# Kernel optimization log

Hardware: AMD Instinct MI355X
Metric: run time of the kernel (lower is better)

The kernel has to match this reference:

```python
import jax, jax.numpy as jnp
import numpy as np

B, S, D_MODEL = 1, 2048, 2048
N_HEADS, N_KV_HEADS, D_HEAD = 16, 4, 128
ROTARY_DIM, ROTARY_BASE = 128, 10000.0
ATTN_SCALE = float(np.sqrt(D_HEAD))
REPEAT = N_HEADS // N_KV_HEADS


def _sin_cos_rotary(n_ctx, rotary_dim, base):
    # TransformerLens calculate_sin_cos_rotary, rotary_adjacent_pairs=False:
    # freq repeated as 'd -> (2 d)'
    pos = jnp.arange(n_ctx, dtype=jnp.float32)
    dim = jnp.arange(rotary_dim // 2, dtype=jnp.float32)
    freq = base ** (dim / (rotary_dim / 2))
    freq = jnp.concatenate([freq, freq])  # (2 d)
    angles = pos[:, None] / freq[None, :]  # [n_ctx, rotary_dim]
    return jnp.sin(angles), jnp.cos(angles)


def _rotate_every_two_half(x):
    # rotate_half for non-adjacent pairs: [-x2, x1]
    d = x.shape[-1]
    return jnp.concatenate([-x[..., d // 2:], x[..., : d // 2]], axis=-1)


def _apply_rotary(x, sin, cos):
    # x: [batch, pos, head, d_head]; sin/cos: [n_ctx, rotary_dim]
    p = x.shape[1]
    s = sin[:p][:, None, :]  # [pos, 1, rotary_dim]
    c = cos[:p][:, None, :]
    x_rot = x[..., :ROTARY_DIM]
    x_pass = x[..., ROTARY_DIM:]
    x_rotated = x_rot * c + _rotate_every_two_half(x_rot) * s
    return jnp.concatenate([x_rotated, x_pass], axis=-1)


def setup_inputs() -> dict:
    key = jax.random.key(0)
    ks = jax.random.split(key, 10)
    init = 1.0 / np.sqrt(D_MODEL)
    return {
        "query_input": jax.random.normal(ks[0], (B, S, D_MODEL), jnp.float32),
        "key_input": jax.random.normal(ks[1], (B, S, D_MODEL), jnp.float32),
        "value_input": jax.random.normal(ks[2], (B, S, D_MODEL), jnp.float32),
        "W_Q": jax.random.normal(ks[3], (N_HEADS, D_MODEL, D_HEAD), jnp.float32) * init,
        "b_Q": jnp.zeros((N_HEADS, D_HEAD), jnp.float32),
        "W_K": jax.random.normal(ks[4], (N_KV_HEADS, D_MODEL, D_HEAD), jnp.float32) * init,
        "b_K": jnp.zeros((N_KV_HEADS, D_HEAD), jnp.float32),
        "W_V": jax.random.normal(ks[5], (N_KV_HEADS, D_MODEL, D_HEAD), jnp.float32) * init,
        "b_V": jnp.zeros((N_KV_HEADS, D_HEAD), jnp.float32),
        "W_O": jax.random.normal(ks[6], (N_HEADS, D_HEAD, D_MODEL), jnp.float32) * init,
        "b_O": jnp.zeros((D_MODEL,), jnp.float32),
    }


def reference(query_input, key_input, value_input, W_Q, b_Q, W_K, b_K, W_V, b_V, W_O, b_O):
    sin, cos = _sin_cos_rotary(S, ROTARY_DIM, ROTARY_BASE)

    # Projections
    q = jnp.einsum("bpd,hdk->bphk", query_input, W_Q) + b_Q   # [B,S,H,dh]
    k = jnp.einsum("bpd,hdk->bphk", key_input, W_K) + b_K     # [B,S,Hkv,dh]
    v = jnp.einsum("bpd,hdk->bphk", value_input, W_V) + b_V   # [B,S,Hkv,dh]

    # Rotary on q and k (before KV head expansion)
    q = _apply_rotary(q, sin, cos)
    k = _apply_rotary(k, sin, cos)

    # GQA expansion via repeat_interleave on head dim
    k = jnp.repeat(k, REPEAT, axis=2)  # [B,S,H,dh]
    v = jnp.repeat(v, REPEAT, axis=2)

    # Attention scores, causal mask, softmax
    scores = jnp.einsum("bqhd,bkhd->bhqk", q, k) / ATTN_SCALE  # [B,H,S,S]
    causal = jnp.tril(jnp.ones((S, S), dtype=bool))
    scores = jnp.where(causal, scores, jnp.finfo(scores.dtype).min)
    pattern = jax.nn.softmax(scores, axis=-1)

    # Weighted values and output projection
    z = jnp.einsum("bhqk,bkhd->bqhd", pattern, v)              # [B,S,H,dh]
    out = jnp.einsum("bqhd,hdm->bqm", z, W_O) + b_O            # [B,S,D]
    return out
```

## Files before the change

### kernel.cpp

```cpp
#include <hip/hip_runtime.h>
#include <hip/hip_bf16.h>
#include <stdint.h>
#include <math.h>

typedef __bf16 bf16_t;
typedef __attribute__((ext_vector_type(8))) __bf16 bf16x8;
typedef __attribute__((ext_vector_type(4))) __bf16 bf16x4;
typedef __attribute__((ext_vector_type(4))) float f32x4;
typedef __attribute__((ext_vector_type(16))) float f32x16;
typedef unsigned int uint2v __attribute__((ext_vector_type(2)));

static constexpr int S = 2048;
static constexpr int DM = 2048;
static constexpr int NH = 16;
static constexpr int NKV = 4;
static constexpr int DH = 128;

#define MFMA16(a, b, c) __builtin_amdgcn_mfma_f32_16x16x32_bf16((a), (b), (c), 0, 0, 0)
#define MFMA32(a, b, c) __builtin_amdgcn_mfma_f32_32x32x16_bf16((a), (b), (c), 0, 0, 0)

__device__ __forceinline__ void gload_lds16(const void* g, void* l) {
  __builtin_amdgcn_global_load_lds((__attribute__((address_space(1))) void*)(g),
                                   (__attribute__((address_space(3))) void*)(l), 16, 0, 0);
}

template <int N>
__device__ __forceinline__ void wait_vmcnt() {
  asm volatile("s_waitcnt vmcnt(%0)" :: "n"(N) : "memory");
}
__device__ __forceinline__ void wait_lgkm0() {
  asm volatile("s_waitcnt lgkmcnt(0)" ::: "memory");
}

__device__ __forceinline__ unsigned cvtpk(float lo, float hi) {
  unsigned r;
  asm("v_cvt_pk_bf16_f32 %0, %1, %2" : "=v"(r) : "v"(lo), "v"(hi));
  return r;
}
__device__ __forceinline__ void plswap2(unsigned& a, unsigned& b) {
  uint2v r = __builtin_amdgcn_permlane32_swap(a, b, false, false);
  a = r[0]; b = r[1];
}
__device__ __forceinline__ float swapred_max(float x) {
  uint2v r = __builtin_amdgcn_permlane32_swap(__float_as_uint(x), __float_as_uint(x), false, false);
  return fmaxf(__uint_as_float(r[0]), __uint_as_float(r[1]));
}
__device__ __forceinline__ float swapred_sum(float x) {
  uint2v r = __builtin_amdgcn_permlane32_swap(__float_as_uint(x), __float_as_uint(x), false, false);
  return __uint_as_float(r[0]) + __uint_as_float(r[1]);
}
__device__ __forceinline__ bf16x8 packfrag(float a0, float a1, float a2, float a3,
                                           float a4, float a5, float a6, float a7) {
  unsigned w0 = cvtpk(a0, a1), w1 = cvtpk(a2, a3);
  unsigned w2 = cvtpk(a4, a5), w3 = cvtpk(a6, a7);
  plswap2(w0, w2); plswap2(w1, w3);
  union { unsigned u[4]; bf16x8 v; } u;
  u.u[0] = w0; u.u[1] = w1; u.u[2] = w2; u.u[3] = w3;
  return u.v;
}

__device__ const unsigned char attn_map[51] = {
  120,121,122,123,124, 112,113,114,115,116, 104,105,106,107, 96,97,98,99,
  88,89,90,91, 80,81,82, 72,73,74, 64,65,66, 56,57, 48,49, 40,41, 32, 24, 16,
  108, 83, 58, 33, 8, 125, 100, 75, 50, 25, 0};
__device__ const unsigned char sbase[16] = {0,0,0,0,2,4,6,9,12,15,19,23,27,32,37,42};

__global__ __launch_bounds__(256)
void prep_k(const float* __restrict__ Xq, const float* __restrict__ Xk,
            const float* __restrict__ Xv, const float* __restrict__ WQ,
            const float* __restrict__ WK, const float* __restrict__ WV,
            const float* __restrict__ WO, float2* __restrict__ tab,
            bf16_t* __restrict__ xq, bf16_t* __restrict__ xk, bf16_t* __restrict__ xv,
            bf16_t* __restrict__ wqT, bf16_t* __restrict__ wkT, bf16_t* __restrict__ wvT,
            bf16_t* __restrict__ woT) {
  __shared__ float tile[32][33];
  const int b = blockIdx.x, t = threadIdx.x;
  if (b < 512) {
    int idx = b * 256 + t;
    int p = idx >> 6, j = idx & 63;
    double inv = exp2(-(double)j * 13.287712379549449 / 64.0);
    double ang = (double)p * inv;
    tab[idx] = make_float2((float)sin(ang), (float)cos(ang));
  } else if (b < 12800) {
    int i = ((b - 512) * 256 + t) * 4;
    const float* in; bf16_t* out; int off;
    if (i < 4194304) { in = Xq; out = xq; off = i; }
    else if (i < 8388608) { in = Xk; out = xk; off = i - 4194304; }
    else { in = Xv; out = xv; off = i - 8388608; }
    f32x4 v = *(const f32x4*)(in + off);
    bf16x4 o;
    o[0] = (bf16_t)v[0]; o[1] = (bf16_t)v[1]; o[2] = (bf16_t)v[2]; o[3] = (bf16_t)v[3];
    *(bf16x4*)(out + off) = o;
  } else if (b < 16896) {
    int b2 = b - 12800;
    int bx = b2 & 3, by = (b2 >> 2) & 63, bz = b2 >> 8;
    int c0 = bx * 32, r0 = by * 32;
    int tx = t & 31, ty = t >> 5;
    const float* src = WQ + (size_t)bz * 2048 * 128;
    #pragma unroll
    for (int j = 0; j < 32; j += 8)
      tile[ty + j][tx] = src[(size_t)(r0 + ty + j) * 128 + c0 + tx];
    __syncthreads();
    #pragma unroll
    for (int j = 0; j < 32; j += 8)
      wqT[(size_t)(bz * 128 + c0 + ty + j) * 2048 + r0 + tx] = (bf16_t)tile[tx][ty + j];
  } else if (b < 18944) {
    int b2 = b - 16896;
    int bx = b2 & 3, by = (b2 >> 2) & 63, bz = b2 >> 8;
    int g = bz & 3;
    const float* in = (bz < 4) ? WK : WV;
    bf16_t* out = (bz < 4) ? wkT : wvT;
    int c0 = bx * 32, r0 = by * 32;
    int tx = t & 31, ty = t >> 5;
    const float* src = in + (size_t)g * 2048 * 128;
    #pragma unroll
    for (int j = 0; j < 32; j += 8)
      tile[ty + j][tx] = src[(size_t)(r0 + ty + j) * 128 + c0 + tx];
    __syncthreads();
    #pragma unroll
    for (int j = 0; j < 32; j += 8)
      out[(size_t)(g * 128 + c0 + ty + j) * 2048 + r0 + tx] = (bf16_t)tile[tx][ty + j];
  } else {
    int b2 = b - 18944;
    int bx = b2 & 63, by = (b2 >> 6) & 3, bz = b2 >> 8;
    int c0 = bx * 32, r0 = by * 32;
    int tx = t & 31, ty = t >> 5;
    const float* src = WO + (size_t)bz * 128 * 2048;
    #pragma unroll
    for (int j = 0; j < 32; j += 8)
      tile[ty + j][tx] = src[(size_t)(r0 + ty + j) * 2048 + c0 + tx];
    __syncthreads();
    #pragma unroll
    for (int j = 0; j < 32; j += 8)
      woT[(size_t)(c0 + ty + j) * 2048 + bz * 128 + r0 + tx] = (bf16_t)tile[tx][ty + j];
  }
}

__global__ __launch_bounds__(256)
void proj_gemm_k(const bf16_t* __restrict__ xq, const bf16_t* __restrict__ xk,
                 const bf16_t* __restrict__ xv, const bf16_t* __restrict__ wqT,
                 const bf16_t* __restrict__ wkT, const bf16_t* __restrict__ wvT,
                 const float* __restrict__ bQ, const float* __restrict__ bK,
                 const float* __restrict__ bV, const float2* __restrict__ tab,
                 float qscale, bf16_t* __restrict__ Qb,
                 bf16_t* __restrict__ Kb, bf16_t* __restrict__ Vt) {
  const int b = blockIdx.x;
  const int xcd = b & 7, idx = b >> 3;
  const int nb = (xcd & 3) * 12 + idx % 12;
  const int m0 = ((xcd >> 2) * 8 + idx / 12) * 128;
  const bf16_t* A; const bf16_t* B; const float* bias; bf16_t* dst;
  int ncol0 = 0, hbase = 0, hb = 0;
  float scale = 1.0f;
  bool vmode = false;
  if (nb < 32)      { A = xq; B = wqT; bias = bQ; dst = Qb; hbase = (nb >> 1) * 128; hb = nb & 1; scale = qscale; }
  else if (nb < 40) { A = xk; B = wkT; bias = bK; dst = Kb; hbase = ((nb - 32) >> 1) * 128; hb = (nb - 32) & 1; }
  else              { A = xv; B = wvT; bias = bV; dst = Vt; ncol0 = (nb - 40) * 64; vmode = true; }
  const int K = 2048;
  const int t = threadIdx.x;
  const int lane = t & 63, w = t >> 6;
  const int l15 = lane & 15, lg = lane >> 4;
  const int wr = (w >> 1) * 64, wc = (w & 1) * 32;

  __shared__ bf16_t lA[2][128 * 64];
  __shared__ bf16_t lB[2][64 * 64];

  f32x4 acc[4][2] = {};
  const int srow = t >> 3;
  const int sslot = t & 7;

  auto stage = [&](int buf, int kt) {
    #pragma unroll
    for (int i = 0; i < 4; ++i) {
      int row = i * 32 + srow;
      int ss = sslot ^ (row & 7);
      gload_lds16(A + (size_t)(m0 + row) * K + kt * 64 + ss * 8,
                  (void*)(&lA[buf][0] + i * 2048 + t * 8));
    }
    #pragma unroll
    for (int i = 0; i < 2; ++i) {
      int row = i * 32 + srow;
      int ss = sslot ^ (row & 7);
      int grow = vmode ? (ncol0 + row)
                       : (hbase + hb * 32 + (row >> 1) + 64 * (row & 1));
      gload_lds16(B + (size_t)grow * K + kt * 64 + ss * 8,
                  (void*)(&lB[buf][0] + i * 2048 + t * 8));
    }
  };

  const int nk = K >> 6;
  stage(0, 0);
  for (int kt = 0; kt < nk; ++kt) {
    const int cur = kt & 1;
    if (kt + 1 < nk) {
      stage(cur ^ 1, kt + 1);
      wait_vmcnt<6>();
    } else {
      wait_vmcnt<0>();
    }
    __builtin_amdgcn_s_barrier();
    #pragma unroll
    for (int kk = 0; kk < 2; ++kk) {
      bf16x8 af[4], bfv[2];
      #pragma unroll
      for (int f = 0; f < 4; ++f) {
        int row = wr + f * 16 + l15;
        int slot = kk * 4 + lg;
        af[f] = *(const bf16x8*)(&lA[cur][0] + row * 64 + ((slot ^ (row & 7)) * 8));
      }
      #pragma unroll
      for (int f = 0; f < 2; ++f) {
        int row = wc + f * 16 + l15;
        int slot = kk * 4 + lg;
        bfv[f] = *(const bf16x8*)(&lB[cur][0] + row * 64 + ((slot ^ (row & 7)) * 8));
      }
      #pragma unroll
      for (int fm = 0; fm < 4; ++fm)
        #pragma unroll
        for (int fn = 0; fn < 2; ++fn)
          acc[fm][fn] = MFMA16(af[fm], bfv[fn], acc[fm][fn]);
    }
    wait_lgkm0();
    __builtin_amdgcn_s_barrier();
  }

  if (vmode) {
    #pragma unroll
    for (int fm = 0; fm < 4; ++fm) {
      int rowb = m0 + wr + fm * 16 + lg * 4;
      #pragma unroll
      for (int fn = 0; fn < 2; ++fn) {
        int col = ncol0 + wc + fn * 16 + l15;
        float bb = bias[col];
        bf16x4 pk;
        #pragma unroll
        for (int r = 0; r < 4; ++r) pk[r] = (bf16_t)(acc[fm][fn][r] + bb);
        *(bf16x4*)(dst + (size_t)col * S + rowb) = pk;
      }
    }
  } else {
    #pragma unroll
    for (int fm = 0; fm < 4; ++fm) {
      int rowb = m0 + wr + fm * 16 + lg * 4;
      #pragma unroll
      for (int fn = 0; fn < 2; ++fn) {
        int tc = wc + fn * 16 + l15;
        int j = hb * 32 + (tc >> 1);
        int half = tc & 1;
        int col = hbase + j + 64 * half;
        float bb = bias[col];
        #pragma unroll
        for (int r = 0; r < 4; ++r) {
          int rr = rowb + r;
          float v = acc[fm][fn][r] + bb;
          float o = __shfl_xor(v, 1);
          float2 sc = tab[rr * 64 + j];
          float res = half ? (v * sc.y + o * sc.x) : (v * sc.y - o * sc.x);
          dst[((size_t)(col >> 7) * S + rr) * DH + (col & 127)] = (bf16_t)(res * scale);
        }
      }
    }
  }
}

__global__ __launch_bounds__(256)
void gemm_o_k(const bf16_t* __restrict__ A, const bf16_t* __restrict__ B,
              const float* __restrict__ bias, float* __restrict__ Cout) {
  const int b = blockIdx.x;
  const int xcd = b & 7, idx = b >> 3;
  const int ncol0 = ((xcd & 3) * 8 + (idx & 7)) * 64;
  const int m0 = (((xcd >> 2) * 8) + (idx >> 3)) * 128;
  const int K = 2048;
  const int t = threadIdx.x;
  const int lane = t & 63, w = t >> 6;
  const int l15 = lane & 15, lg = lane >> 4;
  const int wr = (w >> 1) * 64, wc = (w & 1) * 32;

  __shared__ bf16_t lA[2][128 * 64];
  __shared__ bf16_t lB[2][64 * 64];

  f32x4 acc[4][2] = {};
  const int srow = t >> 3;
  const int sslot = t & 7;

  auto stage = [&](int buf, int kt) {
    #pragma unroll
    for (int i = 0; i < 4; ++i) {
      int row = i * 32 + srow;
      int ss = sslot ^ (row & 7);
      gload_lds16(A + (size_t)(m0 + row) * K + kt * 64 + ss * 8,
                  (void*)(&lA[buf][0] + i * 2048 + t * 8));
    }
    #pragma unroll
    for (int i = 0; i < 2; ++i) {
      int row = i * 32 + srow;
      int ss = sslot ^ (row & 7);
      gload_lds16(B + (size_t)(ncol0 + row) * K + kt * 64 + ss * 8,
                  (void*)(&lB[buf][0] + i * 2048 + t * 8));
    }
  };

  const int nk = K >> 6;
  stage(0, 0);
  for (int kt = 0; kt < nk; ++kt) {
    const int cur = kt & 1;
    if (kt + 1 < nk) {
      stage(cur ^ 1, kt + 1);
      wait_vmcnt<6>();
    } else {
      wait_vmcnt<0>();
    }
    __builtin_amdgcn_s_barrier();
    #pragma unroll
    for (int kk = 0; kk < 2; ++kk) {
      bf16x8 af[4], bfv[2];
      #pragma unroll
      for (int f = 0; f < 4; ++f) {
        int row = wr + f * 16 + l15;
        int slot = kk * 4 + lg;
        af[f] = *(const bf16x8*)(&lA[cur][0] + row * 64 + ((slot ^ (row & 7)) * 8));
      }
      #pragma unroll
      for (int f = 0; f < 2; ++f) {
        int row = wc + f * 16 + l15;
        int slot = kk * 4 + lg;
        bfv[f] = *(const bf16x8*)(&lB[cur][0] + row * 64 + ((slot ^ (row & 7)) * 8));
      }
      #pragma unroll
      for (int fm = 0; fm < 4; ++fm)
        #pragma unroll
        for (int fn = 0; fn < 2; ++fn)
          acc[fm][fn] = MFMA16(af[fm], bfv[fn], acc[fm][fn]);
    }
    wait_lgkm0();
    __builtin_amdgcn_s_barrier();
  }

  #pragma unroll
  for (int fm = 0; fm < 4; ++fm) {
    int rowb = m0 + wr + fm * 16 + lg * 4;
    #pragma unroll
    for (int fn = 0; fn < 2; ++fn) {
      int col = ncol0 + wc + fn * 16 + l15;
      float bb = bias[col];
      #pragma unroll
      for (int r = 0; r < 4; ++r)
        Cout[(size_t)(rowb + r) * DM + col] = acc[fm][fn][r] + bb;
    }
  }
}

__global__ __launch_bounds__(256, 2)
void attn_k(const bf16_t* __restrict__ Q, const bf16_t* __restrict__ K,
            const bf16_t* __restrict__ Vt, bf16_t* __restrict__ Z,
            bf16_t* __restrict__ Opart, float* __restrict__ mpart,
            float* __restrict__ lpart) {
  const int bid = blockIdx.x;
  const int h = bid & 15;
  const int g = bid >> 4;
  const int code = attn_map[g];
  const int qb = code >> 3, ci = code & 7;
  const bool split = qb >= 3;
  const int it0 = 3 * ci;
  const int itend = (3 * ci + 2 < qb) ? (3 * ci + 2) : qb;
  const int q0 = qb * 128;
  const int hkv = h >> 2;
  const int t = threadIdx.x;
  const int lane = t & 63, w = t >> 6;
  const int l31 = lane & 31, hi = lane >> 5;
  const int qrow = q0 + w * 32 + l31;

  __shared__ bf16_t lK[128 * 128];
  __shared__ bf16_t lV[128 * 128];

  bf16x8 qf[8];
  #pragma unroll
  for (int j = 0; j < 8; ++j)
    qf[j] = *(const bf16x8*)(Q + ((size_t)h * S + qrow) * DH + j * 16 + hi * 8);

  auto stageK = [&](int it) {
    #pragma unroll
    for (int i = 0; i < 8; ++i) {
      int row = i * 16 + (t >> 4);
      int ss = (t & 15) ^ (row & 15);
      gload_lds16(K + ((size_t)hkv * S + it * 128 + row) * DH + ss * 8,
                  (void*)(lK + i * 2048 + t * 8));
    }
  };
  auto stageV = [&](int it) {
    #pragma unroll
    for (int i = 0; i < 8; ++i) {
      int row = i * 16 + (t >> 4);
      int ss = (t & 15) ^ (row & 15);
      gload_lds16(Vt + ((size_t)hkv * DH + row) * S + it * 128 + ss * 8,
                  (void*)(lV + i * 2048 + t * 8));
    }
  };

  f32x16 oacc0 = {}, oacc1 = {}, oacc2 = {}, oacc3 = {};
  float m_run = -3.0e3f, l_run = 0.f;
  const int msk = l31 & 15;
  const bf16_t* kb0 = lK + l31 * 128;
  const bf16_t* vb0 = lV + l31 * 128;

  stageK(it0);
  stageV(it0);

  for (int it = it0; it <= itend; ++it) {
    wait_vmcnt<8>();
    __builtin_amdgcn_s_barrier();

    f32x16 s0 = {}, s1 = {}, s2 = {}, s3 = {};
    __builtin_amdgcn_s_setprio(1);
    #pragma unroll
    for (int j = 0; j < 8; ++j) {
      int so = ((j * 2 + hi) ^ msk) * 8;
      bf16x8 k0 = *(const bf16x8*)(kb0 + so);
      bf16x8 k1 = *(const bf16x8*)(kb0 + 32 * 128 + so);
      bf16x8 k2 = *(const bf16x8*)(kb0 + 64 * 128 + so);
      bf16x8 k3 = *(const bf16x8*)(kb0 + 96 * 128 + so);
      s0 = MFMA32(k0, qf[j], s0);
      s1 = MFMA32(k1, qf[j], s1);
      s2 = MFMA32(k2, qf[j], s2);
      s3 = MFMA32(k3, qf[j], s3);
    }
    __builtin_amdgcn_s_setprio(0);
    wait_lgkm0();
    __builtin_amdgcn_s_barrier();
    if (it < itend) stageK(it + 1);

    if (it == qb) {
#define MASKG(SN, N) { \
      _Pragma("unroll") \
      for (int r = 0; r < 16; ++r) { \
        int key = it * 128 + (N) * 32 + (r & 3) + 8 * (r >> 2) + 4 * hi; \
        if (key > qrow) SN[r] = -1e30f; \
      } }
      MASKG(s0, 0) MASKG(s1, 1) MASKG(s2, 2) MASKG(s3, 3)
#undef MASKG
    }

    float mxa = fmaxf(fmaxf(s0[0], s1[0]), fmaxf(s2[0], s3[0]));
    float mxb = fmaxf(fmaxf(s0[1], s1[1]), fmaxf(s2[1], s3[1]));
    float mxc = fmaxf(fmaxf(s0[2], s1[2]), fmaxf(s2[2], s3[2]));
    float mxd = fmaxf(fmaxf(s0[3], s1[3]), fmaxf(s2[3], s3[3]));
    #pragma unroll
    for (int r = 4; r < 16; r += 4) {
      mxa = fmaxf(fmaxf(mxa, fmaxf(s0[r], s1[r])), fmaxf(s2[r], s3[r]));
      mxb = fmaxf(fmaxf(mxb, fmaxf(s0[r+1], s1[r+1])), fmaxf(s2[r+1], s3[r+1]));
      mxc = fmaxf(fmaxf(mxc, fmaxf(s0[r+2], s1[r+2])), fmaxf(s2[r+2], s3[r+2]));
      mxd = fmaxf(fmaxf(mxd, fmaxf(s0[r+3], s1[r+3])), fmaxf(s2[r+3], s3[r+3]));
    }
    float mfull = swapred_max(fmaxf(fmaxf(mxa, mxb), fmaxf(mxc, mxd)));

    float m_new, alpha;
    bool nore = __all(mfull - m_run <= 8.0f);
    if (nore) { m_new = m_run; alpha = 1.0f; }
    else { m_new = fmaxf(m_run, mfull); alpha = exp2f(m_run - m_new); }

    float psa = 0.f, psb = 0.f, psc = 0.f, psd = 0.f;
#define EXPG(SN) { \
    _Pragma("unroll") \
    for (int r = 0; r < 16; r += 4) { \
      SN[r] = exp2f(SN[r] - m_new); psa += SN[r]; \
      SN[r+1] = exp2f(SN[r+1] - m_new); psb += SN[r+1]; \
      SN[r+2] = exp2f(SN[r+2] - m_new); psc += SN[r+2]; \
      SN[r+3] = exp2f(SN[r+3] - m_new); psd += SN[r+3]; \
    } }
    EXPG(s0) EXPG(s1) EXPG(s2) EXPG(s3)
#undef EXPG
    float lt = swapred_sum((psa + psb) + (psc + psd));
    l_run = l_run * alpha + lt;
    m_run = m_new;

    if (!nore) {
      #pragma unroll
      for (int r = 0; r < 16; ++r) {
        int qs = (r & 3) + 8 * (r >> 2) + 4 * hi;
        float ar = __shfl(alpha, qs);
        oacc0[r] *= ar; oacc1[r] *= ar; oacc2[r] *= ar; oacc3[r] *= ar;
      }
    }

    bf16x8 pa[8];
    pa[0] = packfrag(s0[0], s0[1], s0[2], s0[3], s0[4], s0[5], s0[6], s0[7]);
    pa[1] = packfrag(s0[8], s0[9], s0[10], s0[11], s0[12], s0[13], s0[14], s0[15]);
    pa[2] = packfrag(s1[0], s1[1], s1[2], s1[3], s1[4], s1[5], s1[6], s1[7]);
    pa[3] = packfrag(s1[8], s1[9], s1[10], s1[11], s1[12], s1[13], s1[14], s1[15]);
    pa[4] = packfrag(s2[0], s2[1], s2[2], s2[3], s2[4], s2[5], s2[6], s2[7]);
    pa[5] = packfrag(s2[8], s2[9], s2[10], s2[11], s2[12], s2[13], s2[14], s2[15]);
    pa[6] = packfrag(s3[0], s3[1], s3[2], s3[3], s3[4], s3[5], s3[6], s3[7]);
    pa[7] = packfrag(s3[8], s3[9], s3[10], s3[11], s3[12], s3[13], s3[14], s3[15]);

    if (it < itend) { wait_vmcnt<8>(); }
    else            { wait_vmcnt<0>(); }
    __builtin_amdgcn_s_barrier();

    __builtin_amdgcn_s_setprio(1);
    #pragma unroll
    for (int ks = 0; ks < 8; ++ks) {
      int so = ((ks * 2 + hi) ^ msk) * 8;
      bf16x8 v0 = *(const bf16x8*)(vb0 + so);
      bf16x8 v1 = *(const bf16x8*)(vb0 + 32 * 128 + so);
      bf16x8 v2 = *(const bf16x8*)(vb0 + 64 * 128 + so);
      bf16x8 v3 = *(const bf16x8*)(vb0 + 96 * 128 + so);
      oacc0 = MFMA32(pa[ks], v0, oacc0);
      oacc1 = MFMA32(pa[ks], v1, oacc1);
      oacc2 = MFMA32(pa[ks], v2, oacc2);
      oacc3 = MFMA32(pa[ks], v3, oacc3);
    }
    __builtin_amdgcn_s_setprio(0);
    wait_lgkm0();
    __builtin_amdgcn_s_barrier();
    if (it < itend) stageV(it + 1);
  }

  if (!split) {
    float linv = 1.0f / l_run;
    #pragma unroll
    for (int r = 0; r < 16; ++r) {
      int qs = (r & 3) + 8 * (r >> 2) + 4 * hi;
      float lv = __shfl(linv, qs);
      int qg = q0 + w * 32 + qs;
      bf16_t* zp = Z + (size_t)qg * DM + h * DH + l31;
      zp[0]  = (bf16_t)(oacc0[r] * lv);
      zp[32] = (bf16_t)(oacc1[r] * lv);
      zp[64] = (bf16_t)(oacc2[r] * lv);
      zp[96] = (bf16_t)(oacc3[r] * lv);
    }
  } else {
    const int slot = h * 48 + sbase[qb] + ci;
    bf16_t* Op = Opart + (size_t)slot * 16384;
    #pragma unroll
    for (int r = 0; r < 16; ++r) {
      int qs = (r & 3) + 8 * (r >> 2) + 4 * hi;
      bf16_t* op = Op + (w * 32 + qs) * 128 + l31;
      op[0]  = (bf16_t)oacc0[r];
      op[32] = (bf16_t)oacc1[r];
      op[64] = (bf16_t)oacc2[r];
      op[96] = (bf16_t)oacc3[r];
    }
    if (lane < 32) {
      mpart[slot * 128 + w * 32 + l31] = m_run;
      lpart[slot * 128 + w * 32 + l31] = l_run;
    }
  }
}

__global__ void combine_k(const bf16_t* __restrict__ Opart, const float* __restrict__ mpart,
                          const float* __restrict__ lpart, bf16_t* __restrict__ Z) {
  int tid = blockIdx.x * 256 + threadIdx.x;
  int d4 = tid & 31;
  int q = (tid >> 5) & 127;
  int u = tid >> 12;
  int h = u / 13;
  int qb = 3 + (u - h * 13);
  int nc = (qb + 3) / 3;
  int slot0 = h * 48 + sbase[qb];
  float M = -3.0e3f;
  for (int c = 0; c < nc; ++c) M = fmaxf(M, mpart[(slot0 + c) * 128 + q]);
  float L = 0.f;
  float o0 = 0.f, o1 = 0.f, o2 = 0.f, o3 = 0.f;
  for (int c = 0; c < nc; ++c) {
    float a = exp2f(mpart[(slot0 + c) * 128 + q] - M);
    L += a * lpart[(slot0 + c) * 128 + q];
    bf16x4 ov = *(const bf16x4*)(Opart + (size_t)(slot0 + c) * 16384 + q * 128 + d4 * 4);
    o0 += a * (float)ov[0]; o1 += a * (float)ov[1];
    o2 += a * (float)ov[2]; o3 += a * (float)ov[3];
  }
  float inv = 1.0f / L;
  bf16x4 zv;
  zv[0] = (bf16_t)(o0 * inv); zv[1] = (bf16_t)(o1 * inv);
  zv[2] = (bf16_t)(o2 * inv); zv[3] = (bf16_t)(o3 * inv);
  int qg = qb * 128 + q;
  *(bf16x4*)(Z + (size_t)qg * DM + h * DH + d4 * 4) = zv;
}

extern "C" void kernel_launch(void* const* d_in, const int* in_sizes, int n_in,
                              void* d_out, int out_size, void* d_ws, size_t ws_size,
                              hipStream_t stream) {
  (void)in_sizes; (void)n_in; (void)out_size; (void)ws_size;
  const float* Xq = (const float*)d_in[0];
  const float* Xk = (const float*)d_in[1];
  const float* Xv = (const float*)d_in[2];
  const float* WQ = (const float*)d_in[3];
  const float* bQ = (const float*)d_in[4];
  const float* WK = (const float*)d_in[5];
  const float* bK = (const float*)d_in[6];
  const float* WV = (const float*)d_in[7];
  const float* bV = (const float*)d_in[8];
  const float* WO = (const float*)d_in[9];
  const float* bO = (const float*)d_in[10];

  char* w = (char*)d_ws;
  float2* tab = (float2*)w;
  bf16_t* xq  = (bf16_t*)(w + (1 << 20));
  bf16_t* xk  = xq + 4194304;
  bf16_t* xv  = xk + 4194304;
  bf16_t* wqT = xv + 4194304;
  bf16_t* wkT = wqT + 4194304;
  bf16_t* wvT = wkT + 1048576;
  bf16_t* woT = wvT + 1048576;
  bf16_t* Qb  = woT + 4194304;
  bf16_t* Kb  = Qb + 4194304;
  bf16_t* Vtb = Kb + 1048576;
  bf16_t* Zb  = Vtb + 1048576;
  bf16_t* Opart = xq;
  float* mpart = (float*)tab;
  float* lpart = mpart + 768 * 128;

  prep_k<<<dim3(23040), dim3(256), 0, stream>>>(Xq, Xk, Xv, WQ, WK, WV, WO, tab,
                                                xq, xk, xv, wqT, wkT, wvT, woT);

  const float qscale = 1.4426950408889634f / sqrtf(128.0f);
  proj_gemm_k<<<dim3(768), dim3(256), 0, stream>>>(xq, xk, xv, wqT, wkT, wvT,
                                                   bQ, bK, bV, tab, qscale,
                                                   Qb, Kb, Vtb);

  attn_k<<<dim3(816), dim3(256), 0, stream>>>(Qb, Kb, Vtb, Zb, Opart, mpart, lpart);
  combine_k<<<dim3(3328), dim3(256), 0, stream>>>(Opart, mpart, lpart, Zb);

  gemm_o_k<<<dim3(512), dim3(256), 0, stream>>>(Zb, woT, bO, (float*)d_out);
}
```

Before: 138.4 us.

## Read K tiles directly from global memory and double-buffer V in LDS

The attention kernel no longer stages K through shared memory. Each wave now loads its K fragments for the QK^T MFMAs straight from global memory into registers. The freed LDS holds a second V buffer, so the next V tile is prefetched into the alternate buffer while the current one is consumed, and most barriers and vmcnt waits are removed. The aim is less LDS traffic and synchronization and better overlap of V loads. In exchange, every wave reads the whole K tile from global memory, which relies on cache hits and exposes load latency with no prefetch of K. Correctness of the V buffer also depends on implicit in-order vmcnt waits from the K loads.

```diff
diff --git a/kernel.cpp b/kernel.cpp
--- a/kernel.cpp
+++ b/kernel.cpp
@@ -369,64 +369,47 @@
   const int l31 = lane & 31, hi = lane >> 5;
   const int qrow = q0 + w * 32 + l31;
 
-  __shared__ bf16_t lK[128 * 128];
-  __shared__ bf16_t lV[128 * 128];
+  __shared__ bf16_t lV[2][128 * 128];
 
   bf16x8 qf[8];
   #pragma unroll
   for (int j = 0; j < 8; ++j)
     qf[j] = *(const bf16x8*)(Q + ((size_t)h * S + qrow) * DH + j * 16 + hi * 8);
 
-  auto stageK = [&](int it) {
-    #pragma unroll
-    for (int i = 0; i < 8; ++i) {
-      int row = i * 16 + (t >> 4);
-      int ss = (t & 15) ^ (row & 15);
-      gload_lds16(K + ((size_t)hkv * S + it * 128 + row) * DH + ss * 8,
-                  (void*)(lK + i * 2048 + t * 8));
-    }
-  };
-  auto stageV = [&](int it) {
+  auto stageV = [&](int buf, int it) {
     #pragma unroll
     for (int i = 0; i < 8; ++i) {
       int row = i * 16 + (t >> 4);
       int ss = (t & 15) ^ (row & 15);
       gload_lds16(Vt + ((size_t)hkv * DH + row) * S + it * 128 + ss * 8,
-                  (void*)(lV + i * 2048 + t * 8));
+                  (void*)(&lV[buf][0] + i * 2048 + t * 8));
     }
   };
 
   f32x16 oacc0 = {}, oacc1 = {}, oacc2 = {}, oacc3 = {};
   float m_run = -3.0e3f, l_run = 0.f;
   const int msk = l31 & 15;
-  const bf16_t* kb0 = lK + l31 * 128;
-  const bf16_t* vb0 = lV + l31 * 128;
-
-  stageK(it0);
-  stageV(it0);
+
+  stageV(0, it0);
 
   for (int it = it0; it <= itend; ++it) {
-    wait_vmcnt<8>();
-    __builtin_amdgcn_s_barrier();
-
+    const int cur = (it - it0) & 1;
+
+    const bf16_t* kp = K + ((size_t)hkv * S + (size_t)it * 128 + l31) * DH + hi * 8;
     f32x16 s0 = {}, s1 = {}, s2 = {}, s3 = {};
     __builtin_amdgcn_s_setprio(1);
     #pragma unroll
     for (int j = 0; j < 8; ++j) {
-      int so = ((j * 2 + hi) ^ msk) * 8;
-      bf16x8 k0 = *(const bf16x8*)(kb0 + so);
-      bf16x8 k1 = *(const bf16x8*)(kb0 + 32 * 128 + so);
-      bf16x8 k2 = *(const bf16x8*)(kb0 + 64 * 128 + so);
-      bf16x8 k3 = *(const bf16x8*)(kb0 + 96 * 128 + so);
+      bf16x8 k0 = *(const bf16x8*)(kp + j * 16);
+      bf16x8 k1 = *(const bf16x8*)(kp + 32 * DH + j * 16);
+      bf16x8 k2 = *(const bf16x8*)(kp + 64 * DH + j * 16);
+      bf16x8 k3 = *(const bf16x8*)(kp + 96 * DH + j * 16);
       s0 = MFMA32(k0, qf[j], s0);
       s1 = MFMA32(k1, qf[j], s1);
       s2 = MFMA32(k2, qf[j], s2);
       s3 = MFMA32(k3, qf[j], s3);
     }
     __builtin_amdgcn_s_setprio(0);
-    wait_lgkm0();
-    __builtin_amdgcn_s_barrier();
-    if (it < itend) stageK(it + 1);
 
     if (it == qb) {
 #define MASKG(SN, N) { \
@@ -481,6 +464,8 @@
       }
     }
 
+    if (it < itend) stageV(cur ^ 1, it + 1);
+
     bf16x8 pa[8];
     pa[0] = packfrag(s0[0], s0[1], s0[2], s0[3], s0[4], s0[5], s0[6], s0[7]);
     pa[1] = packfrag(s0[8], s0[9], s0[10], s0[11], s0[12], s0[13], s0[14], s0[15]);
@@ -491,10 +476,10 @@
     pa[6] = packfrag(s3[0], s3[1], s3[2], s3[3], s3[4], s3[5], s3[6], s3[7]);
     pa[7] = packfrag(s3[8], s3[9], s3[10], s3[11], s3[12], s3[13], s3[14], s3[15]);
 
-    if (it < itend) { wait_vmcnt<8>(); }
-    else            { wait_vmcnt<0>(); }
+    if (it == it0) { wait_vmcnt<8>(); }
     __builtin_amdgcn_s_barrier();
 
+    const bf16_t* vb0 = &lV[cur][0] + l31 * 128;
     __builtin_amdgcn_s_setprio(1);
     #pragma unroll
     for (int ks = 0; ks < 8; ++ks) {
@@ -511,7 +496,6 @@
     __builtin_amdgcn_s_setprio(0);
     wait_lgkm0();
     __builtin_amdgcn_s_barrier();
-    if (it < itend) stageV(it + 1);
   }
 
   if (!split) {
```

After: 166.3 us. 1.2x slower.

## Fuse split-KV combine into attention via last-block atomic counter

Applied to the files above, without the earlier changes.

Removes the separate combine kernel launch. Each split attention block writes its partial output, max and sum, fences, and atomically bumps a per-(head, query-block) counter that prep_k resets. The last block to arrive merges all partials into Z. This saves a launch and the gap between kernels, but adds fences, an atomic and a serial tail of combine work on a few blocks.

```diff
diff --git a/kernel.cpp b/kernel.cpp
--- a/kernel.cpp
+++ b/kernel.cpp
@@ -72,10 +72,11 @@
             const float* __restrict__ WO, float2* __restrict__ tab,
             bf16_t* __restrict__ xq, bf16_t* __restrict__ xk, bf16_t* __restrict__ xv,
             bf16_t* __restrict__ wqT, bf16_t* __restrict__ wkT, bf16_t* __restrict__ wvT,
-            bf16_t* __restrict__ woT) {
+            bf16_t* __restrict__ woT, unsigned* __restrict__ cnt) {
   __shared__ float tile[32][33];
   const int b = blockIdx.x, t = threadIdx.x;
   if (b < 512) {
+    if (b == 0 && t < 208) cnt[t] = 0;
     int idx = b * 256 + t;
     int p = idx >> 6, j = idx & 63;
     double inv = exp2(-(double)j * 13.287712379549449 / 64.0);
@@ -353,7 +354,7 @@
 void attn_k(const bf16_t* __restrict__ Q, const bf16_t* __restrict__ K,
             const bf16_t* __restrict__ Vt, bf16_t* __restrict__ Z,
             bf16_t* __restrict__ Opart, float* __restrict__ mpart,
-            float* __restrict__ lpart) {
+            float* __restrict__ lpart, unsigned* __restrict__ cnt) {
   const int bid = blockIdx.x;
   const int h = bid & 15;
   const int g = bid >> 4;
@@ -527,52 +528,61 @@
       zp[64] = (bf16_t)(oacc2[r] * lv);
       zp[96] = (bf16_t)(oacc3[r] * lv);
     }
-  } else {
-    const int slot = h * 48 + sbase[qb] + ci;
-    bf16_t* Op = Opart + (size_t)slot * 16384;
-    #pragma unroll
-    for (int r = 0; r < 16; ++r) {
-      int qs = (r & 3) + 8 * (r >> 2) + 4 * hi;
-      bf16_t* op = Op + (w * 32 + qs) * 128 + l31;
-      op[0]  = (bf16_t)oacc0[r];
-      op[32] = (bf16_t)oacc1[r];
-      op[64] = (bf16_t)oacc2[r];
-      op[96] = (bf16_t)oacc3[r];
-    }
-    if (lane < 32) {
-      mpart[slot * 128 + w * 32 + l31] = m_run;
-      lpart[slot * 128 + w * 32 + l31] = l_run;
-    }
-  }
-}
-
-__global__ void combine_k(const bf16_t* __restrict__ Opart, const float* __restrict__ mpart,
-                          const float* __restrict__ lpart, bf16_t* __restrict__ Z) {
-  int tid = blockIdx.x * 256 + threadIdx.x;
-  int d4 = tid & 31;
-  int q = (tid >> 5) & 127;
-  int u = tid >> 12;
-  int h = u / 13;
-  int qb = 3 + (u - h * 13);
-  int nc = (qb + 3) / 3;
-  int slot0 = h * 48 + sbase[qb];
-  float M = -3.0e3f;
-  for (int c = 0; c < nc; ++c) M = fmaxf(M, mpart[(slot0 + c) * 128 + q]);
-  float L = 0.f;
-  float o0 = 0.f, o1 = 0.f, o2 = 0.f, o3 = 0.f;
-  for (int c = 0; c < nc; ++c) {
-    float a = exp2f(mpart[(slot0 + c) * 128 + q] - M);
-    L += a * lpart[(slot0 + c) * 128 + q];
-    bf16x4 ov = *(const bf16x4*)(Opart + (size_t)(slot0 + c) * 16384 + q * 128 + d4 * 4);
-    o0 += a * (float)ov[0]; o1 += a * (float)ov[1];
-    o2 += a * (float)ov[2]; o3 += a * (float)ov[3];
-  }
-  float inv = 1.0f / L;
-  bf16x4 zv;
-  zv[0] = (bf16_t)(o0 * inv); zv[1] = (bf16_t)(o1 * inv);
-  zv[2] = (bf16_t)(o2 * inv); zv[3] = (bf16_t)(o3 * inv);
-  int qg = qb * 128 + q;
-  *(bf16x4*)(Z + (size_t)qg * DM + h * DH + d4 * 4) = zv;
+    return;
+  }
+
+  const int slot0 = h * 48 + sbase[qb];
+  const int slot = slot0 + ci;
+  bf16_t* Op = Opart + (size_t)slot * 16384;
+  #pragma unroll
+  for (int r = 0; r < 16; ++r) {
+    int qs = (r & 3) + 8 * (r >> 2) + 4 * hi;
+    bf16_t* op = Op + (w * 32 + qs) * 128 + l31;
+    op[0]  = (bf16_t)oacc0[r];
+    op[32] = (bf16_t)oacc1[r];
+    op[64] = (bf16_t)oacc2[r];
+    op[96] = (bf16_t)oacc3[r];
+  }
+  if (lane < 32) {
+    mpart[slot * 128 + w * 32 + l31] = m_run;
+    lpart[slot * 128 + w * 32 + l31] = l_run;
+  }
+  __threadfence();
+
+  const int nc = (qb + 3) / 3;
+  const int u = h * 13 + (qb - 3);
+  volatile int* flag = (volatile int*)lK;
+  __syncthreads();
+  if (t == 0) {
+    unsigned old = atomicAdd(&cnt[u], 1u);
+    *flag = (old == (unsigned)(nc - 1)) ? 1 : 0;
+  }
+  __syncthreads();
+  if (*flag == 0) return;
+
+  __threadfence();
+  #pragma unroll 1
+  for (int i = 0; i < 16; ++i) {
+    int tid2 = t + i * 256;
+    int d4 = tid2 & 31;
+    int q = tid2 >> 5;
+    float M = -3.0e3f;
+    for (int c = 0; c < nc; ++c) M = fmaxf(M, mpart[(slot0 + c) * 128 + q]);
+    float L = 0.f, o0 = 0.f, o1 = 0.f, o2 = 0.f, o3 = 0.f;
+    for (int c = 0; c < nc; ++c) {
+      float a = exp2f(mpart[(slot0 + c) * 128 + q] - M);
+      L += a * lpart[(slot0 + c) * 128 + q];
+      bf16x4 ov = *(const bf16x4*)(Opart + (size_t)(slot0 + c) * 16384 + q * 128 + d4 * 4);
+      o0 += a * (float)ov[0]; o1 += a * (float)ov[1];
+      o2 += a * (float)ov[2]; o3 += a * (float)ov[3];
+    }
+    float inv = 1.0f / L;
+    bf16x4 zv;
+    zv[0] = (bf16_t)(o0 * inv); zv[1] = (bf16_t)(o1 * inv);
+    zv[2] = (bf16_t)(o2 * inv); zv[3] = (bf16_t)(o3 * inv);
+    int qg = q0 + q;
+    *(bf16x4*)(Z + (size_t)qg * DM + h * DH + d4 * 4) = zv;
+  }
 }
 
 extern "C" void kernel_launch(void* const* d_in, const int* in_sizes, int n_in,
@@ -604,20 +614,20 @@
   bf16_t* Kb  = Qb + 4194304;
   bf16_t* Vtb = Kb + 1048576;
   bf16_t* Zb  = Vtb + 1048576;
+  unsigned* cnt = (unsigned*)(Zb + 4194304);
   bf16_t* Opart = xq;
   float* mpart = (float*)tab;
   float* lpart = mpart + 768 * 128;
 
   prep_k<<<dim3(23040), dim3(256), 0, stream>>>(Xq, Xk, Xv, WQ, WK, WV, WO, tab,
-                                                xq, xk, xv, wqT, wkT, wvT, woT);
+                                                xq, xk, xv, wqT, wkT, wvT, woT, cnt);
 
   const float qscale = 1.4426950408889634f / sqrtf(128.0f);
   proj_gemm_k<<<dim3(768), dim3(256), 0, stream>>>(xq, xk, xv, wqT, wkT, wvT,
                                                    bQ, bK, bV, tab, qscale,
                                                    Qb, Kb, Vtb);
 
-  attn_k<<<dim3(816), dim3(256), 0, stream>>>(Qb, Kb, Vtb, Zb, Opart, mpart, lpart);
-  combine_k<<<dim3(3328), dim3(256), 0, stream>>>(Opart, mpart, lpart, Zb);
+  attn_k<<<dim3(816), dim3(256), 0, stream>>>(Qb, Kb, Vtb, Zb, Opart, mpart, lpart, cnt);
 
   gemm_o_k<<<dim3(512), dim3(256), 0, stream>>>(Zb, woT, bO, (float*)d_out);
 }
```

After: 267.0 us. 92.9% more time.
